# Kernel tuning notes

Measured on AMD Instinct MI355X. Metric: run time of the kernel, lower is better.

## Reference

```python
import jax, jax.numpy as jnp
import numpy as np

NUM_GROUPS = 32
EPS = 1e-5


def group_norm(x, gamma, beta):
    # x: [B, C, H, W]
    B, C, H, W = x.shape
    xg = x.reshape(B, NUM_GROUPS, C // NUM_GROUPS, H, W)
    mean = jnp.mean(xg, axis=(2, 3, 4), keepdims=True)
    var = jnp.var(xg, axis=(2, 3, 4), keepdims=True)
    xn = ((xg - mean) * jax.lax.rsqrt(var + EPS)).reshape(B, C, H, W)
    return xn * gamma[None, :, None, None] + beta[None, :, None, None]


def setup_inputs() -> dict:
    key = jax.random.key(0)
    ks = jax.random.split(key, 11)
    B, C, H, W = 16, 512, 48, 48
    scale = 1.0 / np.sqrt(C)
    return {
        "x": jax.random.normal(ks[0], (B, C, H, W), dtype=jnp.float32),
        "gn_gamma": jnp.ones((C,), dtype=jnp.float32),
        "gn_beta": jnp.zeros((C,), dtype=jnp.float32),
        "wq": jax.random.normal(ks[1], (C, C), dtype=jnp.float32) * scale,
        "bq": jnp.zeros((C,), dtype=jnp.float32),
        "wk": jax.random.normal(ks[2], (C, C), dtype=jnp.float32) * scale,
        "bk": jnp.zeros((C,), dtype=jnp.float32),
        "wv": jax.random.normal(ks[3], (C, C), dtype=jnp.float32) * scale,
        "bv": jnp.zeros((C,), dtype=jnp.float32),
        "wo": jax.random.normal(ks[4], (C, C), dtype=jnp.float32) * scale,
        "bo": jnp.zeros((C,), dtype=jnp.float32),
    }


def reference(x, gn_gamma, gn_beta, wq, bq, wk, bk, wv, bv, wo, bo):
    B, C, H, W = x.shape
    y = group_norm(x, gn_gamma, gn_beta)
    yf = y.reshape(B, C, H * W)  # [B, C, N]
    # 1x1 convs == per-position channel GEMMs
    q = jnp.einsum('oc,bcn->bon', wq, yf) + bq[None, :, None]
    k = jnp.einsum('oc,bcn->bon', wk, yf) + bk[None, :, None]
    v = jnp.einsum('oc,bcn->bon', wv, yf) + bv[None, :, None]
    # attn[b,i,j] = q[:, :, i] . k[:, :, j], scaled by sqrt(C)
    attn = jnp.einsum('bci,bcj->bij', q, k) / jnp.sqrt(jnp.float32(C))
    attn = jax.nn.softmax(attn, axis=-1)
    # out[b,c,i] = sum_j v[b,c,j] * attn[b,i,j]
    out = jnp.einsum('bcj,bij->bci', v, attn)
    out = jnp.einsum('oc,bcn->bon', wo, out) + bo[None, :, None]
    return out.reshape(B, C, H, W) + x
```

## Files before the change

### kernel.cpp

```cpp
#include <hip/hip_runtime.h>

#define DI __device__ __forceinline__

typedef __attribute__((ext_vector_type(8))) short bf16x8;
typedef __attribute__((ext_vector_type(4))) short s16x4;
typedef __attribute__((ext_vector_type(4))) float f32x4;

DI short f2bf(float f) {
  unsigned u = __builtin_bit_cast(unsigned, f);
  u += 0x7FFFu + ((u >> 16) & 1u);
  return (short)(u >> 16);
}

#define WAITVM(N) asm volatile("s_waitcnt vmcnt(" #N ")" ::: "memory")


__global__ __launch_bounds__(256) void prep_k(
    const float* __restrict__ wq, const float* __restrict__ wk,
    const float* __restrict__ wv, const float* __restrict__ wo,
    short* __restrict__ Wv, short* __restrict__ Wo,
    short* __restrict__ WkT, short* __restrict__ WqT) {
  const int i = blockIdx.x * 256 + threadIdx.x;
  const float sc = 0.04419417382415922f;
  Wv[i] = f2bf(wv[i]);
  const int c = i & 511;
  const int cp = (c & ~63) | ((c & 15) << 2) | ((c >> 4) & 3);
  Wo[(i & ~511) | cp] = f2bf(wo[i]);
  const int tr = (i & 511) * 512 + (i >> 9);
  WkT[tr] = f2bf(wk[i] * sc);
  WqT[tr] = f2bf(wq[i]);
}

__global__ __launch_bounds__(256) void g0_k(const float* __restrict__ wk,
                                            const float* __restrict__ bq,
                                            float* __restrict__ g0) {
  const int c = blockIdx.x * 256 + threadIdx.x;
  float acc = 0.f;
#pragma unroll 8
  for (int o = 0; o < 512; ++o) acc += wk[o * 512 + c] * bq[o];
  g0[c] = acc * 0.04419417382415922f;
}

__global__ __launch_bounds__(256) void gn_stats(const float* __restrict__ x,
                                                float2* __restrict__ stats) {
  const int bg = blockIdx.x;
  const float4* xg = (const float4*)(x + (size_t)bg * 36864);
  float s = 0.f, q = 0.f;
  for (int i = threadIdx.x; i < 9216; i += 256) {
    float4 v = xg[i];
    s += v.x + v.y + v.z + v.w;
    q += v.x * v.x + v.y * v.y + v.z * v.z + v.w * v.w;
  }
#pragma unroll
  for (int d = 1; d < 64; d <<= 1) { s += __shfl_xor(s, d); q += __shfl_xor(q, d); }
  __shared__ float rs[4], rq[4];
  const int w = threadIdx.x >> 6;
  if ((threadIdx.x & 63) == 0) { rs[w] = s; rq[w] = q; }
  __syncthreads();
  if (threadIdx.x == 0) {
    float S = rs[0] + rs[1] + rs[2] + rs[3];
    float Q = rq[0] + rq[1] + rq[2] + rq[3];
    float mean = S * (1.f / 36864.f);
    float var  = Q * (1.f / 36864.f) - mean * mean;
    float2 o; o.x = mean; o.y = rsqrtf(var + 1e-5f);
    stats[bg] = o;
  }
}

__global__ __launch_bounds__(256) void gn_norm_t(
    const float* __restrict__ x, const float2* __restrict__ stats,
    const float* __restrict__ gamma, const float* __restrict__ beta,
    short* __restrict__ yT) {
  __shared__ float ts[64][68];
  const int n0 = blockIdx.x * 64, c0 = blockIdx.y * 64, b = blockIdx.z;
  const int t = threadIdx.x;
  {
    const int cw = t >> 4;
    const int n4 = (t & 15) * 4;
    const float* xb = x + ((size_t)b * 512 + c0) * 2304 + n0;
#pragma unroll
    for (int r4 = 0; r4 < 4; ++r4) {
      const int c = cw + r4 * 16;
      float4 v = *(const float4*)(xb + (size_t)c * 2304 + n4);
      *(float4*)&ts[c][n4] = v;
    }
  }
  __syncthreads();
  {
    const int c4 = t & 15;
    const int nw = t >> 4;
    const int cg = c0 + c4 * 4;
    const float2 ms = stats[b * 32 + (cg >> 4)];
    const float4 gm = *(const float4*)(gamma + cg);
    const float4 bt = *(const float4*)(beta + cg);
    const float a0 = ms.y * gm.x, a1 = ms.y * gm.y, a2 = ms.y * gm.z, a3 = ms.y * gm.w;
    const float d0 = bt.x - ms.x * a0, d1 = bt.y - ms.x * a1,
                d2 = bt.z - ms.x * a2, d3 = bt.w - ms.x * a3;
#pragma unroll
    for (int it = 0; it < 4; ++it) {
      const int no = nw + it * 16;
      const float v0 = ts[c4 * 4 + 0][no], v1 = ts[c4 * 4 + 1][no];
      const float v2 = ts[c4 * 4 + 2][no], v3 = ts[c4 * 4 + 3][no];
      s16x4 o = { f2bf(v0 * a0 + d0), f2bf(v1 * a1 + d1),
                  f2bf(v2 * a2 + d2), f2bf(v3 * a3 + d3) };
      *(s16x4*)(yT + ((size_t)b * 2304 + n0 + no) * 512 + cg) = o;
    }
  }
}

template <int EPI, bool BIASROW, int LDA, int LDB, int KSTEPS>
__global__ __launch_bounds__(256) void gemm_k(
    const short* __restrict__ A, size_t sA,
    const short* __restrict__ Bt, size_t sB,
    void* __restrict__ Dp, size_t sD,
    const float* __restrict__ bias, const float* __restrict__ resid,
    int N, int tilesM, int boff) {
  __shared__ short As[3][128 * 32];
  __shared__ short Bs[3][128 * 32];
  const int ba = blockIdx.y, bb = blockIdx.y + boff;
  int bx = blockIdx.x;
  bx = (bx & 7) * (int)(gridDim.x >> 3) + (bx >> 3);
  const int tm = bx % tilesM, tn = bx / tilesM;
  const int row0 = tm * 128, col0 = tn * 128;
  const int tid = threadIdx.x, lane = tid & 63, w = tid >> 6;
  const int lr = lane & 15, lg = lane >> 4;
  const short* Ab = A + (size_t)ba * sA;
  const short* Bb = Bt + (size_t)bb * sB;
  f32x4 acc[4][4];
  const f32x4 zero = {0.f, 0.f, 0.f, 0.f};
#pragma unroll
  for (int i = 0; i < 4; ++i)
#pragma unroll
    for (int j = 0; j < 4; ++j) acc[i][j] = zero;
  const int wrow = (w & 1) * 64, wcol = (w >> 1) * 64;
  const int sw = (lg ^ ((lr >> 1) & 3)) * 8;

#define GK_STAGE(KS, BUF)                                                      \
  {                                                                            \
    _Pragma("unroll")                                                          \
    for (int j = 0; j < 2; ++j) {                                              \
      const int g = (w * 2 + j) * 64 + lane;            \
      const int ko = (KS) * 32 + (((g & 3) ^ ((g >> 3) & 3)) * 8);             \
      const short* ga = Ab + (size_t)(row0 + (g >> 2)) * LDA + ko;             \
      const short* gb = Bb + (size_t)(col0 + (g >> 2)) * LDB + ko;             \
      __builtin_amdgcn_global_load_lds(                                        \
          (__attribute__((address_space(1))) void*)ga,                         \
          (__attribute__((address_space(3))) void*)&As[BUF][(w * 2 + j) * 512],\
          16, 0, 0);                                                           \
      __builtin_amdgcn_global_load_lds(                                        \
          (__attribute__((address_space(1))) void*)gb,                         \
          (__attribute__((address_space(3))) void*)&Bs[BUF][(w * 2 + j) * 512],\
          16, 0, 0);                                                           \
    }                                                                          \
  }

  GK_STAGE(0, 0);
  GK_STAGE(1, 1);
  GK_STAGE(2, 2);
  int cur = 0;
  for (int ks = 0; ks < KSTEPS; ++ks) {
    if (ks + 2 < KSTEPS)      WAITVM(8);
    else if (ks + 1 < KSTEPS) WAITVM(4);
    else                      WAITVM(0);
    __builtin_amdgcn_sched_barrier(0);
    __builtin_amdgcn_s_barrier();
    bf16x8 af[4], bfr[4];
#pragma unroll
    for (int mi = 0; mi < 4; ++mi)
      af[mi] = *(const bf16x8*)&As[cur][(wrow + mi * 16 + lr) * 32 + sw];
#pragma unroll
    for (int nj = 0; nj < 4; ++nj)
      bfr[nj] = *(const bf16x8*)&Bs[cur][(wcol + nj * 16 + lr) * 32 + sw];
    __builtin_amdgcn_s_setprio(1);
#pragma unroll
    for (int mi = 0; mi < 4; ++mi)
#pragma unroll
      for (int nj = 0; nj < 4; ++nj)
        acc[mi][nj] = __builtin_amdgcn_mfma_f32_16x16x32_bf16(af[mi], bfr[nj], acc[mi][nj], 0, 0, 0);
    __builtin_amdgcn_s_setprio(0);
    __builtin_amdgcn_s_barrier();
    if (ks + 3 < KSTEPS) { GK_STAGE(ks + 3, cur) }
    cur = (cur == 2) ? 0 : cur + 1;
  }
#undef GK_STAGE

  const size_t bD = (size_t)bb * sD;
  if (EPI == 3) {
    const int colpos = col0 + wcol + lr * 4;
    const int jb = colpos >> 5, j5 = colpos & 31;
#pragma unroll
    for (int mi = 0; mi < 4; ++mi) {
#pragma unroll
      for (int r = 0; r < 4; ++r) {
        const int row = row0 + wrow + mi * 16 + lg * 4 + r;
        const float bv = bias[row];
        const int off = (jb * 32 + (row >> 4)) * 512 + ((row & 15) << 5) + j5;
        s16x4 o = { f2bf(acc[mi][0][r] + bv), f2bf(acc[mi][1][r] + bv),
                    f2bf(acc[mi][2][r] + bv), f2bf(acc[mi][3][r] + bv) };
        *(s16x4*)&((short*)Dp)[bD + off] = o;
      }
    }
  } else {
#pragma unroll
    for (int mi = 0; mi < 4; ++mi) {
#pragma unroll
      for (int nj = 0; nj < 4; ++nj) {
        const int col = col0 + wcol + nj * 16 + lr;
#pragma unroll
        for (int r = 0; r < 4; ++r) {
          const int row = row0 + wrow + mi * 16 + lg * 4 + r;
          float v = acc[mi][nj][r];
          if (EPI != 2) v += (BIASROW ? bias[row] : bias[col]);
          const size_t idx = bD + (size_t)row * N + col;
          if (EPI == 1) {
            ((float*)Dp)[idx] = v + resid[idx];
          } else {
            ((short*)Dp)[idx] = f2bf(v);
          }
        }
      }
    }
  }
}

__global__ __launch_bounds__(256) void gemm_s(
    const short* __restrict__ z, const short* __restrict__ yT,
    short* __restrict__ Praw, float* __restrict__ Tsum, int b0) {
  __shared__ short As[3][128 * 32];
  __shared__ short Bs[3][128 * 32];
  const int cb = blockIdx.y;
  const int b = b0 + cb;
  int bx = blockIdx.x;
  { const int xcd = bx & 7, id8 = bx >> 3;
    bx = (xcd < 4 ? xcd * 41 : 164 + (xcd - 4) * 40) + id8; }
  const int tm = bx % 18, tn = bx / 18;
  const int row0 = tm * 128, col0 = tn * 128;
  const int tid = threadIdx.x, lane = tid & 63, w = tid >> 6;
  const int lr = lane & 15, lg = lane >> 4;
  const short* Ab = z + (size_t)b * 2304 * 512;
  const short* Bb = yT + (size_t)b * 2304 * 512;
  f32x4 acc[4][4];
  const f32x4 zero = {0.f, 0.f, 0.f, 0.f};
#pragma unroll
  for (int i = 0; i < 4; ++i)
#pragma unroll
    for (int j = 0; j < 4; ++j) acc[i][j] = zero;
  const int wrow = (w & 1) * 64, wcol = (w >> 1) * 64;
  const int chalf = w >> 1;
  const int sw = (lg ^ ((lr >> 1) & 3)) * 8;

#define GS_STAGE(KS, BUF)                                                      \
  {                                                                            \
    _Pragma("unroll")                                                          \
    for (int j = 0; j < 2; ++j) {                                              \
      const int g = (w * 2 + j) * 64 + lane;                                   \
      const int ko = (KS) * 32 + (((g & 3) ^ ((g >> 3) & 3)) * 8);             \
      const short* ga = Ab + (size_t)(row0 + (g >> 2)) * 512 + ko;             \
      const short* gb = Bb + (size_t)(col0 + (g >> 2)) * 512 + ko;             \
      __builtin_amdgcn_global_load_lds(                                        \
          (__attribute__((address_space(1))) void*)ga,                         \
          (__attribute__((address_space(3))) void*)&As[BUF][(w * 2 + j) * 512],\
          16, 0, 0);                                                           \
      __builtin_amdgcn_global_load_lds(                                        \
          (__attribute__((address_space(1))) void*)gb,                         \
          (__attribute__((address_space(3))) void*)&Bs[BUF][(w * 2 + j) * 512],\
          16, 0, 0);                                                           \
    }                                                                          \
  }

  GS_STAGE(0, 0);
  GS_STAGE(1, 1);
  GS_STAGE(2, 2);
  int cur = 0;
  for (int ks = 0; ks < 16; ++ks) {
    if (ks < 14)      WAITVM(8);
    else if (ks < 15) WAITVM(4);
    else              WAITVM(0);
    __builtin_amdgcn_sched_barrier(0);
    __builtin_amdgcn_s_barrier();
    bf16x8 af[4], bfr[4];
#pragma unroll
    for (int mi = 0; mi < 4; ++mi)
      af[mi] = *(const bf16x8*)&As[cur][(wrow + mi * 16 + lr) * 32 + sw];
#pragma unroll
    for (int nj = 0; nj < 4; ++nj)
      bfr[nj] = *(const bf16x8*)&Bs[cur][(wcol + nj * 16 + lr) * 32 + sw];
    __builtin_amdgcn_s_setprio(1);
#pragma unroll
    for (int mi = 0; mi < 4; ++mi)
#pragma unroll
      for (int nj = 0; nj < 4; ++nj)
        acc[mi][nj] = __builtin_amdgcn_mfma_f32_16x16x32_bf16(af[mi], bfr[nj], acc[mi][nj], 0, 0, 0);
    __builtin_amdgcn_s_setprio(0);
    __builtin_amdgcn_s_barrier();
    if (ks + 3 < 16) { GS_STAGE(ks + 3, cur) }
    cur = (cur == 2) ? 0 : cur + 1;
  }
#undef GS_STAGE
  short* Pp = Praw + ((size_t)(cb * 18 + tn) * 2304 + row0) * 128;
  float* Ts = Tsum + (size_t)(cb * 2304 + row0) * 36 + tn * 2 + chalf;
#pragma unroll
  for (int mi = 0; mi < 4; ++mi) {
#pragma unroll
    for (int r = 0; r < 4; ++r) {
      const int row = wrow + mi * 16 + lg * 4 + r;
      float pv0 = __expf(acc[mi][0][r] - 30.f);
      float pv1 = __expf(acc[mi][1][r] - 30.f);
      float pv2 = __expf(acc[mi][2][r] - 30.f);
      float pv3 = __expf(acc[mi][3][r] - 30.f);
      float sum = pv0 + pv1 + pv2 + pv3;
#pragma unroll
      for (int d = 1; d < 16; d <<= 1) sum += __shfl_xor(sum, d);
      if (lr == 0) Ts[(size_t)row * 36] = sum;
      s16x4 o = { f2bf(pv0), f2bf(pv1), f2bf(pv2), f2bf(pv3) };
      *(s16x4*)(Pp + (size_t)row * 128 + wcol + lr * 4) = o;
    }
  }
}

__global__ __launch_bounds__(256) void sum_k(
    const float* __restrict__ Tsum, float* __restrict__ linv, int nrows) {
  const int r = blockIdx.x * 256 + threadIdx.x;
  if (r >= nrows) return;
  const float* ts = Tsum + (size_t)r * 36;
  float l = 0.f;
#pragma unroll
  for (int t = 0; t < 36; ++t) l += ts[t];
  linv[r] = 1.f / l;
}

__global__ __launch_bounds__(512) void gemm_pv(
    const short* __restrict__ Praw, const float* __restrict__ linv,
    const short* __restrict__ vsrc, short* __restrict__ Dp, int b0) {
  __shared__ short As[3][144 * 32];
  int tm, cb;
  if (gridDim.y == 16) {
    const int id = blockIdx.y * 16 + blockIdx.x;
    const int xcd = id & 7, r = id >> 3;
    cb = xcd * 2 + (r >= 16 ? 1 : 0);
    tm = r & 15;
  } else {
    cb = blockIdx.y; tm = blockIdx.x;
  }
  const int bb = b0 + cb;
  const int row0 = tm * 144;
  const int tid = threadIdx.x, lane = tid & 63, w = tid >> 6;
  const int lr = lane & 15, lg = lane >> 4;
  const short* Ab = Praw + (size_t)cb * 18 * 2304 * 128;
  const short* Bb = vsrc + (size_t)bb * 512 * 2304;
  const short* Bp0 = Bb + (w * 4 + 0) * 512 + lr * 32 + lg * 8;
  const short* Bp1 = Bb + (w * 4 + 1) * 512 + lr * 32 + lg * 8;
  const short* Bp2 = Bb + (w * 4 + 2) * 512 + lr * 32 + lg * 8;
  const short* Bp3 = Bb + (w * 4 + 3) * 512 + lr * 32 + lg * 8;
  f32x4 acc[9][4];
  const f32x4 zero = {0.f, 0.f, 0.f, 0.f};
#pragma unroll
  for (int i = 0; i < 9; ++i)
#pragma unroll
    for (int j = 0; j < 4; ++j) acc[i][j] = zero;
  const int sw = (lg ^ ((lr >> 1) & 3)) * 8;

#define PVA_STAGE(KS, BUF)                                                     \
  {                                                                            \
    const int kt = (KS) >> 2, k32 = ((KS) & 3) * 32;                           \
    {                                                                          \
      const int g = tid;                                                       \
      const short* ga = Ab + ((size_t)kt * 2304 + row0 + (g >> 2)) * 128 +     \
                        k32 + (((g & 3) ^ ((g >> 3) & 3)) * 8);                \
      __builtin_amdgcn_global_load_lds(                                        \
          (__attribute__((address_space(1))) void*)ga,                         \
          (__attribute__((address_space(3))) void*)&As[BUF][w * 512], 16,0,0); \
    }                                                                          \
    if (w == 0) {                                                              \
      const int g = 512 + tid;                                                 \
      const short* ga = Ab + ((size_t)kt * 2304 + row0 + (g >> 2)) * 128 +     \
                        k32 + (((g & 3) ^ ((g >> 3) & 3)) * 8);                \
      __builtin_amdgcn_global_load_lds(                                        \
          (__attribute__((address_space(1))) void*)ga,                         \
          (__attribute__((address_space(3))) void*)&As[BUF][4096], 16, 0, 0);  \
    }                                                                          \
  }

#define PV_BLOAD(KS, BR)                                                       \
  {                                                                            \
    BR[0] = *(const bf16x8*)(Bp0 + (KS) * 16384);                              \
    BR[1] = *(const bf16x8*)(Bp1 + (KS) * 16384);                              \
    BR[2] = *(const bf16x8*)(Bp2 + (KS) * 16384);                              \
    BR[3] = *(const bf16x8*)(Bp3 + (KS) * 16384);                              \
  }

#define PV_ITER(KS, BUSE, BFILL)                                               \
  {                                                                            \
    if ((KS) < 70)       { if (w == 0) WAITVM(12); else WAITVM(10); }          \
    else if ((KS) == 70) { if (w == 0) WAITVM(10); else WAITVM(8); }           \
    else                 WAITVM(4);                                            \
    __builtin_amdgcn_sched_barrier(0);                                         \
    __builtin_amdgcn_s_barrier();                                              \
    bf16x8 af[9];                                                              \
    _Pragma("unroll")                                                          \
    for (int mi = 0; mi < 9; ++mi)                                             \
      af[mi] = *(const bf16x8*)&As[cur][(mi * 16 + lr) * 32 + sw];             \
    __builtin_amdgcn_s_setprio(1);                                             \
    _Pragma("unroll")                                                          \
    for (int mi = 0; mi < 9; ++mi)                                             \
      _Pragma("unroll")                                                        \
      for (int nj = 0; nj < 4; ++nj)                                           \
        acc[mi][nj] = __builtin_amdgcn_mfma_f32_16x16x32_bf16(                 \
            af[mi], BUSE[nj], acc[mi][nj], 0, 0, 0);                           \
    __builtin_amdgcn_s_setprio(0);                                             \
    __builtin_amdgcn_s_barrier();                                              \
    if ((KS) + 2 < 72) PV_BLOAD((KS) + 2, BFILL);                              \
    if ((KS) + 3 < 72) PVA_STAGE((KS) + 3, cur);                               \
    cur = (cur == 2) ? 0 : cur + 1;                                            \
  }

  bf16x8 bA[4], bB[4];
  PVA_STAGE(0, 0);
  PVA_STAGE(1, 1);
  PVA_STAGE(2, 2);
  PV_BLOAD(0, bA);
  PV_BLOAD(1, bB);
  int cur = 0;
  for (int ks = 0; ks < 72; ks += 2) {
    PV_ITER(ks, bA, bA);
    PV_ITER(ks + 1, bB, bB);
  }
#undef PV_ITER
#undef PV_BLOAD
#undef PVA_STAGE

  const float* lv = linv + (size_t)cb * 2304 + row0;
  short* Db = Dp + (size_t)bb * 2304 * 512;
#pragma unroll
  for (int mi = 0; mi < 9; ++mi) {
#pragma unroll
    for (int r = 0; r < 4; ++r) {
      const int row = mi * 16 + lg * 4 + r;
      const float s = lv[row];
      s16x4 o = { f2bf(acc[mi][0][r] * s), f2bf(acc[mi][1][r] * s),
                  f2bf(acc[mi][2][r] * s), f2bf(acc[mi][3][r] * s) };
      *(s16x4*)(Db + (size_t)(row0 + row) * 512 + w * 64 + lr * 4) = o;
    }
  }
}

extern "C" void kernel_launch(void* const* d_in, const int* in_sizes, int n_in,
                              void* d_out, int out_size, void* d_ws, size_t ws_size,
                              hipStream_t stream) {
  const float* x     = (const float*)d_in[0];
  const float* gamma = (const float*)d_in[1];
  const float* beta  = (const float*)d_in[2];
  const float* wq    = (const float*)d_in[3];
  const float* bq    = (const float*)d_in[4];
  const float* wk    = (const float*)d_in[5];
  const float* wv    = (const float*)d_in[7];
  const float* bv    = (const float*)d_in[8];
  const float* wo    = (const float*)d_in[9];
  const float* bo    = (const float*)d_in[10];

  char* ws = (char*)d_ws;
  float2* stats = (float2*)(ws + 0);
  short*  Wv    = (short*)(ws + 8192);
  short*  Wo    = (short*)(ws + 532480);
  short*  WkT   = (short*)(ws + 1056768);
  short*  WqT   = (short*)(ws + 1581056);
  short*  G     = (short*)(ws + 2105344);
  float*  g0    = (float*)(ws + 2629632);
  short*  yT    = (short*)(ws + 2631680);
  short*  zoT   = (short*)(ws + 40380416);
  short*  vbuf  = (short*)(ws + 78129152);
  short*  Praw  = (short*)(ws + 115877888);
  float*  out   = (float*)d_out;

  const size_t base = 115877888ull;
  const size_t per  = 10616832ull + 331776ull + 9216ull;
  int CH = 16;
  if (ws_size < base + 16 * per) CH = (ws_size >= base + 8 * per) ? 8 : 4;
  float* Tsum = (float*)(ws + base + (size_t)CH * 10616832ull);
  float* linv = (float*)(ws + base + (size_t)CH * (10616832ull + 331776ull));

  const size_t sBN = (size_t)2304 * 512;

  prep_k<<<1024, 256, 0, stream>>>(wq, wk, wv, wo, Wv, Wo, WkT, WqT);
  g0_k<<<2, 256, 0, stream>>>(wk, bq, g0);
  gn_stats<<<512, 256, 0, stream>>>(x, stats);
  gn_norm_t<<<dim3(36, 8, 16), 256, 0, stream>>>(x, stats, gamma, beta, yT);
  gemm_k<2, false, 512, 512, 16><<<dim3(16, 1), 256, 0, stream>>>(
      WkT, 0, WqT, 0, G, 0, nullptr, nullptr, 512, 4, 0);
  gemm_k<3, true, 512, 512, 16><<<dim3(72, 16), 256, 0, stream>>>(
      Wv, 0, yT, sBN, vbuf, sBN, bv, nullptr, 2304, 4, 0);
  gemm_k<0, false, 512, 512, 16><<<dim3(72, 16), 256, 0, stream>>>(
      yT, sBN, G, 0, zoT, sBN, g0, nullptr, 512, 18, 0);

  for (int b0 = 0; b0 < 16; b0 += CH) {
    const int n = (16 - b0 < CH) ? (16 - b0) : CH;
    gemm_s<<<dim3(324, n), 256, 0, stream>>>(zoT, yT, Praw, Tsum, b0);
    sum_k<<<(n * 2304 + 255) / 256, 256, 0, stream>>>(Tsum, linv, n * 2304);
    gemm_pv<<<dim3(16, n), 512, 0, stream>>>(Praw, linv, vbuf, zoT, b0);
  }
  gemm_k<1, true, 512, 512, 16><<<dim3(72, 16), 256, 0, stream>>>(
      Wo, 0, zoT, sBN, out, (size_t)512 * 2304, bo, x, 2304, 4, 0);
}
```

Baseline: 441.8 us.

## Store bf16 operands in 128x32 tiled blocks for contiguous GEMM tile loads

Changes the global layout of yT, zoT, G, Wv and Wo from row-major to a tiled layout of 128-row by 32-column blocks, so each K-step tile a GEMM block loads is one contiguous 8 KB chunk. The producers (prep, group-norm transpose, GEMM epilogues, PV epilogue) write in the tiled layout, and the GEMM loaders use new template flags to address it. The goal is more coalesced, page-friendly global-to-LDS loads. In exchange, epilogue stores become more scattered. The gemm_s and gemm_pv loaders must agree with the new layout, and part of that code is not visible here.

```diff
diff --git a/kernel.cpp b/kernel.cpp
--- a/kernel.cpp
+++ b/kernel.cpp
@@ -22,11 +22,11 @@
     short* __restrict__ WkT, short* __restrict__ WqT) {
   const int i = blockIdx.x * 256 + threadIdx.x;
   const float sc = 0.04419417382415922f;
-  Wv[i] = f2bf(wv[i]);
-  const int c = i & 511;
+  const int o = i >> 9, c = i & 511;
+  Wv[(o >> 7) * 65536 + (c >> 5) * 4096 + (o & 127) * 32 + (c & 31)] = f2bf(wv[i]);
   const int cp = (c & ~63) | ((c & 15) << 2) | ((c >> 4) & 3);
-  Wo[(i & ~511) | cp] = f2bf(wo[i]);
-  const int tr = (i & 511) * 512 + (i >> 9);
+  Wo[(o >> 7) * 65536 + (cp >> 5) * 4096 + (o & 127) * 32 + (cp & 31)] = f2bf(wo[i]);
+  const int tr = c * 512 + o;
   WkT[tr] = f2bf(wk[i] * sc);
   WqT[tr] = f2bf(wq[i]);
 }
@@ -99,16 +99,19 @@
 #pragma unroll
     for (int it = 0; it < 4; ++it) {
       const int no = nw + it * 16;
+      const int n = n0 + no;
       const float v0 = ts[c4 * 4 + 0][no], v1 = ts[c4 * 4 + 1][no];
       const float v2 = ts[c4 * 4 + 2][no], v3 = ts[c4 * 4 + 3][no];
       s16x4 o = { f2bf(v0 * a0 + d0), f2bf(v1 * a1 + d1),
                   f2bf(v2 * a2 + d2), f2bf(v3 * a3 + d3) };
-      *(s16x4*)(yT + ((size_t)b * 2304 + n0 + no) * 512 + cg) = o;
+      *(s16x4*)(yT + (size_t)b * 2304 * 512 + (n >> 7) * 65536 +
+                (cg >> 5) * 4096 + (n & 127) * 32 + (cg & 31)) = o;
     }
   }
 }
 
-template <int EPI, bool BIASROW, int LDA, int LDB, int KSTEPS>
+template <int EPI, bool BIASROW, bool AT, bool BT, bool DT, int LDA, int LDB,
+          int KSTEPS>
 __global__ __launch_bounds__(256) void gemm_k(
     const short* __restrict__ A, size_t sA,
     const short* __restrict__ Bt, size_t sB,
@@ -140,9 +143,15 @@
     _Pragma("unroll")                                                          \
     for (int j = 0; j < 2; ++j) {                                              \
       const int g = (w * 2 + j) * 64 + lane;            \
-      const int ko = (KS) * 32 + (((g & 3) ^ ((g >> 3) & 3)) * 8);             \
-      const short* ga = Ab + (size_t)(row0 + (g >> 2)) * LDA + ko;             \
-      const short* gb = Bb + (size_t)(col0 + (g >> 2)) * LDB + ko;             \
+      const int sub8 = ((g & 3) ^ ((g >> 3) & 3)) * 8;                         \
+      const short* ga = AT ? (Ab + (size_t)row0 * 512 + (KS) * 4096 +          \
+                              (g >> 2) * 32 + sub8)                            \
+                           : (Ab + (size_t)(row0 + (g >> 2)) * LDA +           \
+                              (KS) * 32 + sub8);                               \
+      const short* gb = BT ? (Bb + (size_t)col0 * 512 + (KS) * 4096 +          \
+                              (g >> 2) * 32 + sub8)                            \
+                           : (Bb + (size_t)(col0 + (g >> 2)) * LDB +           \
+                              (KS) * 32 + sub8);                               \
       __builtin_amdgcn_global_load_lds(                                        \
           (__attribute__((address_space(1))) void*)ga,                         \
           (__attribute__((address_space(3))) void*)&As[BUF][(w * 2 + j) * 512],\
@@ -211,10 +220,14 @@
           const int row = row0 + wrow + mi * 16 + lg * 4 + r;
           float v = acc[mi][nj][r];
           if (EPI != 2) v += (BIASROW ? bias[row] : bias[col]);
-          const size_t idx = bD + (size_t)row * N + col;
           if (EPI == 1) {
+            const size_t idx = bD + (size_t)row * N + col;
             ((float*)Dp)[idx] = v + resid[idx];
           } else {
+            const size_t idx = bD + (DT
+                ? (size_t)((row >> 7) * 65536 + (col >> 5) * 4096 +
+                           (row & 127) * 32 + (col & 31))
+                : (size_t)row * N + col);
             ((short*)Dp)[idx] = f2bf(v);
           }
         }
@@ -254,9 +267,11 @@
     _Pragma("unroll")                                                          \
     for (int j = 0; j < 2; ++j) {                                              \
       const int g = (w * 2 + j) * 64 + lane;                                   \
-      const int ko = (KS) * 32 + (((g & 3) ^ ((g >> 3) & 3)) * 8);             \
-      const short* ga = Ab + (size_t)(row0 + (g >> 2)) * 512 + ko;             \
-      const short* gb = Bb + (size_t)(col0 + (g >> 2)) * 512 + ko;             \
+      const int sub8 = ((g & 3) ^ ((g >> 3) & 3)) * 8;                         \
+      const short* ga = Ab + (size_t)row0 * 512 + (KS) * 4096 +                \
+                        (g >> 2) * 32 + sub8;                                  \
+      const short* gb = Bb + (size_t)col0 * 512 + (KS) * 4096 +                \
+                        (g >> 2) * 32 + sub8;                                  \
       __builtin_amdgcn_global_load_lds(                                        \
           (__attribute__((address_space(1))) void*)ga,                         \
           (__attribute__((address_space(3))) void*)&As[BUF][(w * 2 + j) * 512],\
@@ -431,15 +446,18 @@
 
   const float* lv = linv + (size_t)cb * 2304 + row0;
   short* Db = Dp + (size_t)bb * 2304 * 512;
+  const int col = w * 64 + lr * 4;
+  const int coff = (col >> 5) * 4096 + (col & 31);
 #pragma unroll
   for (int mi = 0; mi < 9; ++mi) {
 #pragma unroll
     for (int r = 0; r < 4; ++r) {
       const int row = mi * 16 + lg * 4 + r;
       const float s = lv[row];
+      const int R = row0 + row;
       s16x4 o = { f2bf(acc[mi][0][r] * s), f2bf(acc[mi][1][r] * s),
                   f2bf(acc[mi][2][r] * s), f2bf(acc[mi][3][r] * s) };
-      *(s16x4*)(Db + (size_t)(row0 + row) * 512 + w * 64 + lr * 4) = o;
+      *(s16x4*)(Db + (R >> 7) * 65536 + coff + (R & 127) * 32) = o;
     }
   }
 }
@@ -485,11 +503,11 @@
   g0_k<<<2, 256, 0, stream>>>(wk, bq, g0);
   gn_stats<<<512, 256, 0, stream>>>(x, stats);
   gn_norm_t<<<dim3(36, 8, 16), 256, 0, stream>>>(x, stats, gamma, beta, yT);
-  gemm_k<2, false, 512, 512, 16><<<dim3(16, 1), 256, 0, stream>>>(
+  gemm_k<2, false, false, false, true, 512, 512, 16><<<dim3(16, 1), 256, 0, stream>>>(
       WkT, 0, WqT, 0, G, 0, nullptr, nullptr, 512, 4, 0);
-  gemm_k<3, true, 512, 512, 16><<<dim3(72, 16), 256, 0, stream>>>(
+  gemm_k<3, true, true, true, false, 512, 512, 16><<<dim3(72, 16), 256, 0, stream>>>(
       Wv, 0, yT, sBN, vbuf, sBN, bv, nullptr, 2304, 4, 0);
-  gemm_k<0, false, 512, 512, 16><<<dim3(72, 16), 256, 0, stream>>>(
+  gemm_k<0, false, true, true, true, 512, 512, 16><<<dim3(72, 16), 256, 0, stream>>>(
       yT, sBN, G, 0, zoT, sBN, g0, nullptr, 512, 18, 0);
 
   for (int b0 = 0; b0 < 16; b0 += CH) {
@@ -498,6 +516,6 @@
     sum_k<<<(n * 2304 + 255) / 256, 256, 0, stream>>>(Tsum, linv, n * 2304);
     gemm_pv<<<dim3(16, n), 512, 0, stream>>>(Praw, linv, vbuf, zoT, b0);
   }
-  gemm_k<1, true, 512, 512, 16><<<dim3(72, 16), 256, 0, stream>>>(
+  gemm_k<1, true, true, true, false, 512, 512, 16><<<dim3(72, 16), 256, 0, stream>>>(
       Wo, 0, zoT, sBN, out, (size_t)512 * 2304, bo, x, 2304, 4, 0);
 }
```

Measured after the change: 429.7 us. -2.7%, faster.
